# Performance work log

Measured on AMD Instinct MI355X. Metric: run time of the kernel, lower is better.

Reference implementation:

```python
import jax, jax.numpy as jnp
import numpy as np

N = 100001          # 1000 DAGs * (99 tasks + 1 summary) + 1 global node
E = 3200000
IN_DIM = 8
H = 64
N_DAGS = 1000
TEMPERATURE = 1.0


def setup_inputs() -> dict:
    key = jax.random.key(0)
    ks = jax.random.split(key, 12)
    x = jax.random.normal(ks[0], (N, IN_DIM), dtype=jnp.float32)
    flags = jax.random.bernoulli(ks[1], 0.5, (N,)).astype(jnp.float32)
    x = x.at[:, -1].set(flags)  # last feature column is the schedule flag
    edge_index = jax.random.randint(ks[2], (2, E), 0, N, dtype=jnp.int32)
    dag_summary_index = jnp.arange(N_DAGS, dtype=jnp.int32) * 100 + 99

    def w(k, shape, fan_in):
        return jax.random.normal(k, shape, dtype=jnp.float32) / np.float32(np.sqrt(fan_in))

    return {
        'x': x,
        'edge_index': edge_index,
        'dag_summary_index': dag_summary_index,
        'W1': w(ks[3], (IN_DIM, H), IN_DIM), 'b1': jnp.zeros((H,), jnp.float32),
        'W2': w(ks[4], (H, H), H),           'b2': jnp.zeros((H,), jnp.float32),
        'M1': w(ks[5], (3 * H, H), 3 * H),   'mb1': jnp.zeros((H,), jnp.float32),
        'M2': w(ks[6], (H, H), H),           'mb2': jnp.zeros((H,), jnp.float32),
        'M3': w(ks[7], (H, 1), H),           'mb3': jnp.zeros((1,), jnp.float32),
    }


def _gcn_conv(x, src, dst, W, b):
    # PyG GCNConv: add self-loops, symmetric normalization, linear, scatter-add, bias
    n = x.shape[0]
    loop = jnp.arange(n, dtype=src.dtype)
    s = jnp.concatenate([src, loop])
    d = jnp.concatenate([dst, loop])
    deg = jax.ops.segment_sum(jnp.ones_like(s, dtype=x.dtype), d, num_segments=n)
    dinv = jnp.where(deg > 0, jax.lax.rsqrt(deg), 0.0)
    norm = dinv[s] * dinv[d]                      # [E+N]
    h = x @ W                                     # [N, H]
    msg = h[s] * norm[:, None]                    # gather + scale (memory-bound)
    return jax.ops.segment_sum(msg, d, num_segments=n) + b


def reference(x, edge_index, dag_summary_index, W1, b1, W2, b2, M1, mb1, M2, mb2, M3, mb3):
    src, dst = edge_index[0], edge_index[1]
    h = jax.nn.relu(_gcn_conv(x, src, dst, W1, b1))
    h = jax.nn.relu(_gcn_conv(h, src, dst, W2, b2))   # [N, H]

    n = x.shape[0]
    idx = jnp.arange(n - 1)
    # dag_idx for node i == number of summary indices <= i (matches loop increment)
    dag_of = jnp.searchsorted(dag_summary_index, idx, side='right')
    dag_of = jnp.clip(dag_of, 0, dag_summary_index.shape[0] - 1)
    dag_emb = h[dag_summary_index[dag_of]]            # [N-1, H]
    global_emb = jnp.broadcast_to(h[-1], (n - 1, h.shape[1]))
    combined = jnp.concatenate([h[:-1], dag_emb, global_emb], axis=1)  # [N-1, 3H]

    z = jax.nn.relu(combined @ M1 + mb1)
    z = jax.nn.relu(z @ M2 + mb2)
    scores = (z @ M3 + mb3)[:, 0]                     # [N-1]

    flags = x[:-1, -1]
    is_summary = jnp.zeros((n,), bool).at[dag_summary_index].set(True)[:-1]
    mask = (flags == 1.0) & (~is_summary)
    probs = jax.nn.softmax(jnp.where(mask, scores / TEMPERATURE, -jnp.inf))
    selected = jnp.argmax(probs)                      # is_sampling=False path
    return probs, selected
```

## Files before the change

kernel.cpp:

```cpp
#include <hip/hip_runtime.h>
#include <math.h>

#define CHUNK 8192
#define BSTRIDE 17408


__global__ void __launch_bounds__(256) k_bscatter1p(const int* __restrict__ src,
                                                    const int* __restrict__ dst, int e,
                                                    int* __restrict__ bcur,
                                                    unsigned* __restrict__ eu) {
    __shared__ unsigned short rank[CHUNK];
    __shared__ int cnt[256];
    __shared__ int base[256];
    int t = threadIdx.x;
    int c0 = blockIdx.x * CHUNK;
    cnt[t] = 0;
    __syncthreads();
#pragma unroll
    for (int k = 0; k < CHUNK / 256; k++) {
        int i = c0 + k * 256 + t;
        if (i < e) {
            int b = dst[i] >> 9;
            rank[k * 256 + t] = (unsigned short)atomicAdd(&cnt[b], 1);
        }
    }
    __syncthreads();
    int cb = cnt[t];
    base[t] = cb ? atomicAdd(&bcur[t], cb) : 0;
    __syncthreads();
#pragma unroll
    for (int k = 0; k < CHUNK / 256; k++) {
        int i = c0 + k * 256 + t;
        if (i < e) {
            int d = dst[i];
            int b = d >> 9;
            eu[(size_t)b * BSTRIDE + base[b] + rank[k * 256 + t]] =
                ((unsigned)src[i] << 9) | (unsigned)(d & 511);
        }
    }
}

__global__ void __launch_bounds__(256) k_bprep(const unsigned* __restrict__ eu,
                                               const int* __restrict__ bcur,
                                               const float* __restrict__ x,
                                               int* __restrict__ deg, int* __restrict__ off,
                                               float* __restrict__ dinv, float* __restrict__ xs,
                                               int* __restrict__ csr, int n) {
    __shared__ int h[512];
    __shared__ int offL[512];
    __shared__ int curL[512];
    __shared__ float sdv[512];
    int t = threadIdx.x, b = blockIdx.x;
    h[t] = 0; h[t + 256] = 0;
    curL[t] = 0; curL[t + 256] = 0;
    __syncthreads();
    int s0 = b * BSTRIDE;
    int s1 = s0 + bcur[b];
    for (int i = s0 + t; i < s1; i += 256)
        atomicAdd(&h[eu[i] & 511u], 1);
    __syncthreads();
    int o0 = h[t], o1 = h[t + 256];
    for (int d = 1; d < 512; d <<= 1) {
        int a0 = (t >= d) ? h[t - d] : 0;
        int a1 = (t + 256 >= d) ? h[t + 256 - d] : 0;
        __syncthreads();
        h[t] += a0; h[t + 256] += a1;
        __syncthreads();
    }
    int nbase = b << 9;
    int n0 = nbase + t, n1 = nbase + t + 256;
    int ofA = s0 + h[t] - o0, ofB = s0 + h[t + 256] - o1;
    offL[t] = ofA; offL[t + 256] = ofB;
    if (n0 < n) {
        float dv = rsqrtf((float)(o0 + 1));
        deg[n0] = o0; off[n0] = ofA; dinv[n0] = dv; sdv[t] = dv;
    }
    if (n1 < n) {
        float dv = rsqrtf((float)(o1 + 1));
        deg[n1] = o1; off[n1] = ofB; dinv[n1] = dv; sdv[t + 256] = dv;
    }
    __syncthreads();
    int limit = (n - nbase) * 8;
    if (limit > 4096) limit = 4096;
    for (int idx = t; idx < limit; idx += 256)
        xs[(size_t)nbase * 8 + idx] = x[(size_t)nbase * 8 + idx] * sdv[idx >> 3];
    for (int i = s0 + t; i < s1; i += 256) {
        unsigned p = eu[i];
        int local = (int)(p & 511u);
        int r = atomicAdd(&curL[local], 1);
        csr[offL[local] + r] = (int)(p >> 9);
    }
}


__global__ void __launch_bounds__(256) k_conv8(const float* __restrict__ xs,
                                               const int* __restrict__ csr,
                                               const int* __restrict__ off,
                                               const int* __restrict__ deg,
                                               float* __restrict__ agg1, int n) {
    int g = (blockIdx.x * 256 + threadIdx.x) >> 3;
    int lane = threadIdx.x & 7;
    if (g >= n) return;
    int base = off[g], cnt = deg[g];
    float acc = xs[g * 8 + lane];
    int e = 0;
    for (; e + 4 <= cnt; e += 4) {
        int s0 = csr[base + e];
        int s1 = csr[base + e + 1];
        int s2 = csr[base + e + 2];
        int s3 = csr[base + e + 3];
        acc += xs[s0 * 8 + lane];
        acc += xs[s1 * 8 + lane];
        acc += xs[s2 * 8 + lane];
        acc += xs[s3 * 8 + lane];
    }
    for (; e < cnt; e++) acc += xs[csr[base + e] * 8 + lane];
    agg1[g * 8 + lane] = acc;
}


__global__ void k_h1(const float* __restrict__ agg1, const float* __restrict__ W1,
                     const float* __restrict__ b1, const float* __restrict__ dinv,
                     float* __restrict__ H1s, int n) {
    int t = blockIdx.x * blockDim.x + threadIdx.x;
    int i = t >> 6, j = t & 63;
    if (i >= n) return;
    const float* ar = agg1 + (size_t)i * 8;
    float acc = 0.f;
#pragma unroll
    for (int k = 0; k < 8; k++) acc += ar[k] * W1[k * 64 + j];
    float dv = dinv[i];
    float h = fmaxf(dv * acc + b1[j], 0.f);
    H1s[(size_t)i * 64 + j] = h * dv;
}


__global__ void __launch_bounds__(256) k_conv64(const float* __restrict__ G,
                                                const int* __restrict__ csr,
                                                const int* __restrict__ off,
                                                const int* __restrict__ deg,
                                                float* __restrict__ agg2, int n) {
    int d = (blockIdx.x * 256 + threadIdx.x) >> 6;
    int j = threadIdx.x & 63;
    if (d >= n) return;
    int du = __builtin_amdgcn_readfirstlane(d);
    int base = off[du], cnt = deg[du];
    const float* Gj = G + j;
    float acc = Gj[(size_t)du * 64];
    int e = 0;
    for (; e + 8 <= cnt; e += 8) {
        int s[8];
#pragma unroll
        for (int u = 0; u < 8; u++) s[u] = csr[base + e + u];
        float v[8];
#pragma unroll
        for (int u = 0; u < 8; u++) v[u] = Gj[(size_t)s[u] * 64];
#pragma unroll
        for (int u = 0; u < 8; u++) acc += v[u];
    }
    for (; e < cnt; e++) acc += Gj[(size_t)csr[base + e] * 64];
    agg2[(size_t)d * 64 + j] = acc;
}


__global__ void k_dgt2(const float* __restrict__ agg2, const int* __restrict__ dsi,
                       const float* __restrict__ dinv,
                       const float* __restrict__ W2, const float* __restrict__ b2,
                       const float* __restrict__ M1, const float* __restrict__ b1,
                       float* __restrict__ dgt, int n, int nd) {
    int w = (blockIdx.x * blockDim.x + threadIdx.x) >> 6;
    int lane = threadIdx.x & 63;
    if (w >= nd) return;
    int nodeD = dsi[w];
    float avD = agg2[(size_t)nodeD * 64 + lane];
    float dvD = dinv[nodeD];
    float avG = agg2[(size_t)(n - 1) * 64 + lane];
    float dvG = dinv[n - 1];
    float sD = 0.f, sG = 0.f;
#pragma unroll
    for (int k = 0; k < 64; k++) {
        float wv = W2[k * 64 + lane];
        sD += __shfl(avD, k) * wv;
        sG += __shfl(avG, k) * wv;
    }
    float bb = b2[lane];
    float hd = fmaxf(dvD * sD + bb, 0.f);
    float hg = fmaxf(dvG * sG + bb, 0.f);
    float z = b1[lane];
#pragma unroll
    for (int k = 0; k < 64; k++) z += __shfl(hd, k) * M1[(64 + k) * 64 + lane];
#pragma unroll
    for (int k = 0; k < 64; k++) z += __shfl(hg, k) * M1[(128 + k) * 64 + lane];
    dgt[w * 64 + lane] = z;
}


__global__ void __launch_bounds__(256) k_gm(const float* __restrict__ agg2,
                                            const float* __restrict__ dinv,
                                            const float* __restrict__ W2,
                                            const float* __restrict__ b2,
                                            const float* __restrict__ dgt,
                                            const float* __restrict__ x,
                                            const float* __restrict__ M1,
                                            const float* __restrict__ M2,
                                            const float* __restrict__ mb2,
                                            const float* __restrict__ M3,
                                            const float* __restrict__ mb3,
                                            float* __restrict__ scores, int n, int nd) {
    __shared__ float hs[128 * 65];
    __shared__ float ws[64 * 64];
    int tid = threadIdx.x;
    int base = blockIdx.x * 128;
#pragma unroll
    for (int m = 0; m < 4; m++) {
        int i = (m * 256 + tid) * 4;
        *(float4*)&ws[i] = *(const float4*)&W2[i];
    }
#pragma unroll
    for (int m = 0; m < 8; m++) {
        int idx = (m * 256 + tid) * 4;
        int node = idx >> 6, k = idx & 63;
        float4 v = *(const float4*)&agg2[(size_t)(base + node) * 64 + k];
        hs[node * 65 + k]     = v.x;
        hs[node * 65 + k + 1] = v.y;
        hs[node * 65 + k + 2] = v.z;
        hs[node * 65 + k + 3] = v.w;
    }
    __syncthreads();
    int jg = tid & 7, ng = tid >> 3;
    int j0 = jg * 8, n0 = ng * 4;
    float acc[4][8];
#pragma unroll
    for (int i = 0; i < 4; i++)
#pragma unroll
        for (int j = 0; j < 8; j++) acc[i][j] = 0.f;
#pragma unroll 4
    for (int k = 0; k < 64; k++) {
        float av[4];
#pragma unroll
        for (int i = 0; i < 4; i++) av[i] = hs[(n0 + i) * 65 + k];
        float bv[8];
        *(float4*)&bv[0] = *(float4*)&ws[k * 64 + j0];
        *(float4*)&bv[4] = *(float4*)&ws[k * 64 + j0 + 4];
#pragma unroll
        for (int i = 0; i < 4; i++)
#pragma unroll
            for (int j = 0; j < 8; j++) acc[i][j] += av[i] * bv[j];
    }
    __syncthreads();
    float b2v[8];
    *(float4*)&b2v[0] = *(const float4*)&b2[j0];
    *(float4*)&b2v[4] = *(const float4*)&b2[j0 + 4];
#pragma unroll
    for (int i = 0; i < 4; i++) {
        int node = base + n0 + i;
        float dv = (node < n) ? dinv[node] : 0.f;
#pragma unroll
        for (int j = 0; j < 8; j++)
            hs[(n0 + i) * 65 + j0 + j] = fmaxf(acc[i][j] * dv + b2v[j], 0.f);
    }
#pragma unroll
    for (int m = 0; m < 4; m++) {
        int i = (m * 256 + tid) * 4;
        *(float4*)&ws[i] = *(const float4*)&M1[i];
    }
    __syncthreads();
#pragma unroll
    for (int i = 0; i < 4; i++)
#pragma unroll
        for (int j = 0; j < 8; j++) acc[i][j] = 0.f;
#pragma unroll 4
    for (int k = 0; k < 64; k++) {
        float av[4];
#pragma unroll
        for (int i = 0; i < 4; i++) av[i] = hs[(n0 + i) * 65 + k];
        float bv[8];
        *(float4*)&bv[0] = *(float4*)&ws[k * 64 + j0];
        *(float4*)&bv[4] = *(float4*)&ws[k * 64 + j0 + 4];
#pragma unroll
        for (int i = 0; i < 4; i++)
#pragma unroll
            for (int j = 0; j < 8; j++) acc[i][j] += av[i] * bv[j];
    }
    __syncthreads();
#pragma unroll
    for (int i = 0; i < 4; i++) {
        int node = base + n0 + i;
        int dago = (node + 1) / 100;
        if (dago >= nd) dago = nd - 1;
        float dv[8];
        *(float4*)&dv[0] = *(const float4*)&dgt[dago * 64 + j0];
        *(float4*)&dv[4] = *(const float4*)&dgt[dago * 64 + j0 + 4];
#pragma unroll
        for (int j = 0; j < 8; j++)
            hs[(n0 + i) * 65 + j0 + j] = fmaxf(acc[i][j] + dv[j], 0.f);
    }
#pragma unroll
    for (int m = 0; m < 4; m++) {
        int i = (m * 256 + tid) * 4;
        *(float4*)&ws[i] = *(const float4*)&M2[i];
    }
    __syncthreads();
    float acc2[4][8];
#pragma unroll
    for (int i = 0; i < 4; i++)
#pragma unroll
        for (int j = 0; j < 8; j++) acc2[i][j] = 0.f;
#pragma unroll 4
    for (int k = 0; k < 64; k++) {
        float av[4];
#pragma unroll
        for (int i = 0; i < 4; i++) av[i] = hs[(n0 + i) * 65 + k];
        float bv[8];
        *(float4*)&bv[0] = *(float4*)&ws[k * 64 + j0];
        *(float4*)&bv[4] = *(float4*)&ws[k * 64 + j0 + 4];
#pragma unroll
        for (int i = 0; i < 4; i++)
#pragma unroll
            for (int j = 0; j < 8; j++) acc2[i][j] += av[i] * bv[j];
    }
    float mb2v[8], m3v[8];
    *(float4*)&mb2v[0] = *(const float4*)&mb2[j0];
    *(float4*)&mb2v[4] = *(const float4*)&mb2[j0 + 4];
    *(float4*)&m3v[0] = *(const float4*)&M3[j0];
    *(float4*)&m3v[4] = *(const float4*)&M3[j0 + 4];
    float b3 = mb3[0];
#pragma unroll
    for (int i = 0; i < 4; i++) {
        float p = 0.f;
#pragma unroll
        for (int j = 0; j < 8; j++) {
            float z2 = fmaxf(acc2[i][j] + mb2v[j], 0.f);
            p += z2 * m3v[j];
        }
        p += __shfl_xor(p, 1);
        p += __shfl_xor(p, 2);
        p += __shfl_xor(p, 4);
        if (jg == 0) {
            int node = base + n0 + i;
            if (node < n - 1) {
                float flag = x[(size_t)node * 8 + 7];
                bool summary = ((node % 100) == 99);
                scores[node] = (flag == 1.0f && !summary) ? (p + b3) : -INFINITY;
            }
        }
    }
}


__global__ void k_red_ms(const float* __restrict__ scores, int n,
                         float* __restrict__ pm, float* __restrict__ ps,
                         int* __restrict__ pidx) {
    __shared__ float sm[256];
    __shared__ float ss[256];
    __shared__ int si[256];
    float m = -INFINITY, s = 0.f;
    int bi = 0x7fffffff;
    for (int i = blockIdx.x * 256 + threadIdx.x; i < n; i += gridDim.x * 256) {
        float v = scores[i];
        if (v > m) {
            s = s * expf(m - v) + 1.f;
            m = v;
            bi = i;
        } else if (v != -INFINITY) {
            s += expf(v - m);
        }
    }
    sm[threadIdx.x] = m; ss[threadIdx.x] = s; si[threadIdx.x] = bi;
    __syncthreads();
    for (int o = 128; o; o >>= 1) {
        if (threadIdx.x < o) {
            float m2 = sm[threadIdx.x + o], s2 = ss[threadIdx.x + o];
            int i2 = si[threadIdx.x + o];
            float m1 = sm[threadIdx.x], s1 = ss[threadIdx.x];
            int i1 = si[threadIdx.x];
            float M = fmaxf(m1, m2);
            float S = ((m1 == -INFINITY) ? 0.f : s1 * expf(m1 - M)) +
                      ((m2 == -INFINITY) ? 0.f : s2 * expf(m2 - M));
            int I;
            if (m2 > m1 || (m2 == m1 && i2 < i1)) I = i2; else I = i1;
            sm[threadIdx.x] = M; ss[threadIdx.x] = S; si[threadIdx.x] = I;
        }
        __syncthreads();
    }
    if (threadIdx.x == 0) { pm[blockIdx.x] = sm[0]; ps[blockIdx.x] = ss[0]; pidx[blockIdx.x] = si[0]; }
}

__global__ void k_red_comb(const float* __restrict__ pm, const float* __restrict__ ps,
                           const int* __restrict__ pidx, int nb,
                           float* __restrict__ finals, int* __restrict__ seli) {
    __shared__ float sm[256];
    __shared__ float ss[256];
    __shared__ int si[256];
    int t = threadIdx.x;
    sm[t] = (t < nb) ? pm[t] : -INFINITY;
    ss[t] = (t < nb) ? ps[t] : 0.f;
    si[t] = (t < nb) ? pidx[t] : 0x7fffffff;
    __syncthreads();
    for (int o = 128; o; o >>= 1) {
        if (t < o) {
            float m2 = sm[t + o], s2 = ss[t + o];
            int i2 = si[t + o];
            float m1 = sm[t], s1 = ss[t];
            int i1 = si[t];
            float M = fmaxf(m1, m2);
            float S = ((m1 == -INFINITY) ? 0.f : s1 * expf(m1 - M)) +
                      ((m2 == -INFINITY) ? 0.f : s2 * expf(m2 - M));
            int I;
            if (m2 > m1 || (m2 == m1 && i2 < i1)) I = i2; else I = i1;
            sm[t] = M; ss[t] = S; si[t] = I;
        }
        __syncthreads();
    }
    if (t == 0) { finals[0] = sm[0]; finals[1] = ss[0]; seli[0] = si[0]; }
}

__global__ void k_probs(const float* __restrict__ scores, const float* __restrict__ finals,
                        const int* __restrict__ seli, float* __restrict__ out, int n) {
    int i = blockIdx.x * 256 + threadIdx.x;
    float m = finals[0];
    float s = finals[1];
    if (i < n) out[i] = expf(scores[i] - m) / s;
    if (i == 0) out[n] = (float)seli[0];
}


extern "C" void kernel_launch(void* const* d_in, const int* in_sizes, int n_in,
                              void* d_out, int out_size, void* d_ws, size_t ws_size,
                              hipStream_t stream) {
    const float* x   = (const float*)d_in[0];
    const int*   ei  = (const int*)d_in[1];
    const int*   dsi = (const int*)d_in[2];
    const float* W1  = (const float*)d_in[3];
    const float* b1  = (const float*)d_in[4];
    const float* W2  = (const float*)d_in[5];
    const float* b2  = (const float*)d_in[6];
    const float* M1  = (const float*)d_in[7];
    const float* mb1 = (const float*)d_in[8];  (void)mb1;
    const float* M2  = (const float*)d_in[9];
    const float* mb2 = (const float*)d_in[10];
    const float* M3  = (const float*)d_in[11];
    const float* mb3 = (const float*)d_in[12];

    int N  = in_sizes[0] / 8;
    int E  = in_sizes[1] / 2;
    int ND = in_sizes[2];

    int NPAD = ((N + 127) / 128) * 128;
    int TILES = NPAD / 128;
    int nb = (N + 511) >> 9;
    size_t EST = (size_t)nb * BSTRIDE;

    char* p = (char*)d_ws;
    auto alloc = [&](size_t bytes) {
        char* r = p;
        p += (bytes + 255) & ~(size_t)255;
        return r;
    };
    int*   deg    = (int*)alloc((size_t)NPAD * 4);
    int*   off    = (int*)alloc((size_t)NPAD * 4);
    float* dinv   = (float*)alloc((size_t)NPAD * 4);
    int*   csr    = (int*)alloc(EST * 4);
    float* A      = (float*)alloc((size_t)NPAD * 64 * 4);
    float* B      = (float*)alloc((size_t)NPAD * 64 * 4);
    float* xs     = (float*)alloc((size_t)NPAD * 8 * 4);
    float* agg1   = (float*)alloc((size_t)NPAD * 8 * 4);
    float* dgt    = (float*)alloc((size_t)ND * 64 * 4);
    float* scores = (float*)alloc((size_t)NPAD * 4);
    int*   bcur   = (int*)alloc(256 * 4);
    float* pm     = (float*)alloc(256 * 4);
    float* ps     = (float*)alloc(256 * 4);
    int*   pidx   = (int*)alloc(256 * 4);
    float* finals = (float*)alloc(16 * 4);
    int*   seli   = (int*)alloc(16 * 4);
    if ((size_t)(p - (char*)d_ws) > ws_size) return;

    unsigned* eu = (unsigned*)A;

    const int* esrc = ei;
    const int* edst = ei + E;

    hipMemsetAsync(bcur, 0, 256 * 4, stream);
    k_bscatter1p<<<(E + CHUNK - 1) / CHUNK, 256, 0, stream>>>(esrc, edst, E, bcur, eu);
    k_bprep<<<nb, 256, 0, stream>>>(eu, bcur, x, deg, off, dinv, xs, csr, N);

    k_conv8<<<(N * 8 + 255) / 256, 256, 0, stream>>>(xs, csr, off, deg, agg1, N);
    k_h1<<<(N * 64 + 255) / 256, 256, 0, stream>>>(agg1, W1, b1, dinv, A, N);

    k_conv64<<<(N + 3) / 4, 256, 0, stream>>>(A, csr, off, deg, B, N);

    k_dgt2<<<(ND * 64 + 255) / 256, 256, 0, stream>>>(B, dsi, dinv, W2, b2, M1, b1, dgt, N, ND);
    k_gm<<<TILES, 256, 0, stream>>>(B, dinv, W2, b2, dgt, x, M1, M2, mb2, M3, mb3, scores, N, ND);

    int NS = N - 1;
    k_red_ms<<<256, 256, 0, stream>>>(scores, NS, pm, ps, pidx);
    k_red_comb<<<1, 256, 0, stream>>>(pm, ps, pidx, 256, finals, seli);
    k_probs<<<(NS + 256) / 256, 256, 0, stream>>>(scores, finals, seli, (float*)d_out, NS);
}
```

Before: 298.3 us.

## Count degrees with global atomics in scatter pass and fuse conv8 with H1 transform

```diff
diff --git a/kernel.cpp b/kernel.cpp
--- a/kernel.cpp
+++ b/kernel.cpp
@@ -8,6 +8,7 @@
 __global__ void __launch_bounds__(256) k_bscatter1p(const int* __restrict__ src,
                                                     const int* __restrict__ dst, int e,
                                                     int* __restrict__ bcur,
+                                                    int* __restrict__ degG,
                                                     unsigned* __restrict__ eu) {
     __shared__ unsigned short rank[CHUNK];
     __shared__ int cnt[256];
@@ -20,8 +21,9 @@
     for (int k = 0; k < CHUNK / 256; k++) {
         int i = c0 + k * 256 + t;
         if (i < e) {
-            int b = dst[i] >> 9;
-            rank[k * 256 + t] = (unsigned short)atomicAdd(&cnt[b], 1);
+            int d = dst[i];
+            atomicAdd(&degG[d], 1);
+            rank[k * 256 + t] = (unsigned short)atomicAdd(&cnt[d >> 9], 1);
         }
     }
     __syncthreads();
@@ -40,26 +42,24 @@
     }
 }
 
-__global__ void __launch_bounds__(256) k_bprep(const unsigned* __restrict__ eu,
-                                               const int* __restrict__ bcur,
-                                               const float* __restrict__ x,
-                                               int* __restrict__ deg, int* __restrict__ off,
-                                               float* __restrict__ dinv, float* __restrict__ xs,
-                                               int* __restrict__ csr, int n) {
+__global__ void __launch_bounds__(256) k_bprep2(const unsigned* __restrict__ eu,
+                                                const int* __restrict__ bcur,
+                                                const int* __restrict__ degG,
+                                                const float* __restrict__ x,
+                                                int* __restrict__ off,
+                                                float* __restrict__ dinv, float* __restrict__ xs,
+                                                int* __restrict__ csr, int n) {
     __shared__ int h[512];
-    __shared__ int offL[512];
     __shared__ int curL[512];
     __shared__ float sdv[512];
     int t = threadIdx.x, b = blockIdx.x;
-    h[t] = 0; h[t + 256] = 0;
+    int nbase = b << 9;
+    int n0 = nbase + t, n1 = nbase + t + 256;
+    int d0 = (n0 < n) ? degG[n0] : 0;
+    int d1 = (n1 < n) ? degG[n1] : 0;
+    h[t] = d0; h[t + 256] = d1;
     curL[t] = 0; curL[t + 256] = 0;
     __syncthreads();
-    int s0 = b * BSTRIDE;
-    int s1 = s0 + bcur[b];
-    for (int i = s0 + t; i < s1; i += 256)
-        atomicAdd(&h[eu[i] & 511u], 1);
-    __syncthreads();
-    int o0 = h[t], o1 = h[t + 256];
     for (int d = 1; d < 512; d <<= 1) {
         int a0 = (t >= d) ? h[t - d] : 0;
         int a1 = (t + 256 >= d) ? h[t + 256 - d] : 0;
@@ -67,39 +67,50 @@
         h[t] += a0; h[t + 256] += a1;
         __syncthreads();
     }
-    int nbase = b << 9;
-    int n0 = nbase + t, n1 = nbase + t + 256;
-    int ofA = s0 + h[t] - o0, ofB = s0 + h[t + 256] - o1;
-    offL[t] = ofA; offL[t + 256] = ofB;
+    int s0 = b * BSTRIDE;
+    int ofA = s0 + h[t] - d0, ofB = s0 + h[t + 256] - d1;
     if (n0 < n) {
-        float dv = rsqrtf((float)(o0 + 1));
-        deg[n0] = o0; off[n0] = ofA; dinv[n0] = dv; sdv[t] = dv;
+        float dv = rsqrtf((float)(d0 + 1));
+        off[n0] = ofA; dinv[n0] = dv; sdv[t] = dv;
     }
     if (n1 < n) {
-        float dv = rsqrtf((float)(o1 + 1));
-        deg[n1] = o1; off[n1] = ofB; dinv[n1] = dv; sdv[t + 256] = dv;
-    }
-    __syncthreads();
+        float dv = rsqrtf((float)(d1 + 1));
+        off[n1] = ofB; dinv[n1] = dv; sdv[t + 256] = dv;
+    }
+    __syncthreads();
+    h[t] = ofA; h[t + 256] = ofB;
     int limit = (n - nbase) * 8;
     if (limit > 4096) limit = 4096;
     for (int idx = t; idx < limit; idx += 256)
         xs[(size_t)nbase * 8 + idx] = x[(size_t)nbase * 8 + idx] * sdv[idx >> 3];
+    __syncthreads();
+    int s1 = s0 + bcur[b];
     for (int i = s0 + t; i < s1; i += 256) {
         unsigned p = eu[i];
         int local = (int)(p & 511u);
         int r = atomicAdd(&curL[local], 1);
-        csr[offL[local] + r] = (int)(p >> 9);
-    }
-}
-
-
-__global__ void __launch_bounds__(256) k_conv8(const float* __restrict__ xs,
-                                               const int* __restrict__ csr,
-                                               const int* __restrict__ off,
-                                               const int* __restrict__ deg,
-                                               float* __restrict__ agg1, int n) {
-    int g = (blockIdx.x * 256 + threadIdx.x) >> 3;
-    int lane = threadIdx.x & 7;
+        csr[h[local] + r] = (int)(p >> 9);
+    }
+}
+
+
+__global__ void __launch_bounds__(256) k_c8h1(const float* __restrict__ xs,
+                                              const int* __restrict__ csr,
+                                              const int* __restrict__ off,
+                                              const int* __restrict__ deg,
+                                              const float* __restrict__ W1,
+                                              const float* __restrict__ b1,
+                                              const float* __restrict__ dinv,
+                                              float* __restrict__ H1s, int n) {
+    __shared__ float w1s[512];
+    __shared__ float b1s[64];
+    int t = threadIdx.x;
+    w1s[t] = W1[t];
+    w1s[t + 256] = W1[t + 256];
+    if (t < 64) b1s[t] = b1[t];
+    __syncthreads();
+    int g = (blockIdx.x * 256 + t) >> 3;
+    int lane = t & 7;
     if (g >= n) return;
     int base = off[g], cnt = deg[g];
     float acc = xs[g * 8 + lane];
@@ -115,23 +126,27 @@
         acc += xs[s3 * 8 + lane];
     }
     for (; e < cnt; e++) acc += xs[csr[base + e] * 8 + lane];
-    agg1[g * 8 + lane] = acc;
-}
-
-
-__global__ void k_h1(const float* __restrict__ agg1, const float* __restrict__ W1,
-                     const float* __restrict__ b1, const float* __restrict__ dinv,
-                     float* __restrict__ H1s, int n) {
-    int t = blockIdx.x * blockDim.x + threadIdx.x;
-    int i = t >> 6, j = t & 63;
-    if (i >= n) return;
-    const float* ar = agg1 + (size_t)i * 8;
-    float acc = 0.f;
-#pragma unroll
-    for (int k = 0; k < 8; k++) acc += ar[k] * W1[k * 64 + j];
-    float dv = dinv[i];
-    float h = fmaxf(dv * acc + b1[j], 0.f);
-    H1s[(size_t)i * 64 + j] = h * dv;
+    float dv = dinv[g];
+    float o[8];
+#pragma unroll
+    for (int j = 0; j < 8; j++) o[j] = 0.f;
+#pragma unroll
+    for (int k = 0; k < 8; k++) {
+        float av = __shfl(acc, (t & 56) | k);
+#pragma unroll
+        for (int j = 0; j < 8; j++) o[j] += av * w1s[k * 64 + lane * 8 + j];
+    }
+    float4 r0, r1;
+    r0.x = fmaxf(dv * o[0] + b1s[lane * 8 + 0], 0.f) * dv;
+    r0.y = fmaxf(dv * o[1] + b1s[lane * 8 + 1], 0.f) * dv;
+    r0.z = fmaxf(dv * o[2] + b1s[lane * 8 + 2], 0.f) * dv;
+    r0.w = fmaxf(dv * o[3] + b1s[lane * 8 + 3], 0.f) * dv;
+    r1.x = fmaxf(dv * o[4] + b1s[lane * 8 + 4], 0.f) * dv;
+    r1.y = fmaxf(dv * o[5] + b1s[lane * 8 + 5], 0.f) * dv;
+    r1.z = fmaxf(dv * o[6] + b1s[lane * 8 + 6], 0.f) * dv;
+    r1.w = fmaxf(dv * o[7] + b1s[lane * 8 + 7], 0.f) * dv;
+    *(float4*)&H1s[(size_t)g * 64 + lane * 8]     = r0;
+    *(float4*)&H1s[(size_t)g * 64 + lane * 8 + 4] = r1;
 }
 
 
@@ -457,6 +472,7 @@
         p += (bytes + 255) & ~(size_t)255;
         return r;
     };
+    int*   bcur   = (int*)alloc(256 * 4);
     int*   deg    = (int*)alloc((size_t)NPAD * 4);
     int*   off    = (int*)alloc((size_t)NPAD * 4);
     float* dinv   = (float*)alloc((size_t)NPAD * 4);
@@ -464,10 +480,8 @@
     float* A      = (float*)alloc((size_t)NPAD * 64 * 4);
     float* B      = (float*)alloc((size_t)NPAD * 64 * 4);
     float* xs     = (float*)alloc((size_t)NPAD * 8 * 4);
-    float* agg1   = (float*)alloc((size_t)NPAD * 8 * 4);
     float* dgt    = (float*)alloc((size_t)ND * 64 * 4);
     float* scores = (float*)alloc((size_t)NPAD * 4);
-    int*   bcur   = (int*)alloc(256 * 4);
     float* pm     = (float*)alloc(256 * 4);
     float* ps     = (float*)alloc(256 * 4);
     int*   pidx   = (int*)alloc(256 * 4);
@@ -480,12 +494,11 @@
     const int* esrc = ei;
     const int* edst = ei + E;
 
-    hipMemsetAsync(bcur, 0, 256 * 4, stream);
-    k_bscatter1p<<<(E + CHUNK - 1) / CHUNK, 256, 0, stream>>>(esrc, edst, E, bcur, eu);
-    k_bprep<<<nb, 256, 0, stream>>>(eu, bcur, x, deg, off, dinv, xs, csr, N);
-
-    k_conv8<<<(N * 8 + 255) / 256, 256, 0, stream>>>(xs, csr, off, deg, agg1, N);
-    k_h1<<<(N * 64 + 255) / 256, 256, 0, stream>>>(agg1, W1, b1, dinv, A, N);
+    hipMemsetAsync(bcur, 0, 1024 + (size_t)NPAD * 4, stream);
+    k_bscatter1p<<<(E + CHUNK - 1) / CHUNK, 256, 0, stream>>>(esrc, edst, E, bcur, deg, eu);
+    k_bprep2<<<nb, 256, 0, stream>>>(eu, bcur, deg, x, off, dinv, xs, csr, N);
+
+    k_c8h1<<<(N * 8 + 255) / 256, 256, 0, stream>>>(xs, csr, off, deg, W1, b1, dinv, A, N);
 
     k_conv64<<<(N + 3) / 4, 256, 0, stream>>>(A, csr, off, deg, B, N);
 
```

New measurement: 388.7 us. +30.3%, slower.
